# Performance work log

Measured on AMD Instinct MI355X. Metric: run time of the kernel, lower is better.

## Reference

```python
import jax, jax.numpy as jnp
import numpy as np

N = 50000
E = 800000
IN_F, HID, OUT_F = 512, 256, 64
KEEP = 0.5  # Dropout(0.5)


def setup_inputs() -> dict:
    key = jax.random.key(0)
    ks = jax.random.split(key, 7)
    X = jax.random.normal(ks[0], (N, IN_F), dtype=jnp.float32)
    # Xavier-uniform-style init for the two layer weights
    lim1 = float(np.sqrt(6.0 / (IN_F + HID)))
    lim2 = float(np.sqrt(6.0 / (HID + OUT_F)))
    W1 = jax.random.uniform(ks[1], (IN_F, HID), jnp.float32, -lim1, lim1)
    W2 = jax.random.uniform(ks[2], (HID, OUT_F), jnp.float32, -lim2, lim2)
    a_row = jnp.sort(jax.random.randint(ks[3], (E,), 0, N)).astype(jnp.int64)
    a_col = jax.random.randint(ks[4], (E,), 0, N).astype(jnp.int64)
    a_val = jax.random.uniform(ks[5], (E,), jnp.float32)
    drop_mask = jax.random.randint(ks[6], (N, HID), 0, 2).astype(jnp.int32)
    return {"X": X, "W1": W1, "W2": W2, "a_row": a_row, "a_col": a_col,
            "a_val": a_val, "drop_mask": drop_mask}


def _spmm(a_row, a_col, a_val, dense):
    # A @ dense where A is [N, N] sparse in COO form: gather + weighted segment-sum
    msgs = a_val[:, None] * dense[a_col]          # [E, d]
    return jax.ops.segment_sum(msgs, a_row, num_segments=N)


def reference(X, W1, W2, a_row, a_col, a_val, drop_mask):
    # layer 1: feature transform + neighbor aggregation
    h = _spmm(a_row, a_col, a_val, X @ W1)        # [N, HID]
    h = jax.nn.relu(h)
    h = h * drop_mask.astype(h.dtype) * (1.0 / KEEP)  # Dropout(0.5), train mode
    # layer 2
    out = _spmm(a_row, a_col, a_val, h @ W2)      # [N, OUT_F]
    return jax.nn.log_softmax(out, axis=1)
```

## Files before the change

### kernel.cpp

```cpp
#include <hip/hip_runtime.h>
#include <hip/hip_fp16.h>
#include <math.h>

#define NN   50000
#define EE   800000
#define INF  512
#define HIDF 256
#define OUTF 64
#define MTILES (NN/16)

using half8  = __attribute__((ext_vector_type(8))) _Float16;
using half2v = __attribute__((ext_vector_type(2))) _Float16;
using f32x4  = __attribute__((ext_vector_type(4))) float;

#if __has_builtin(__builtin_amdgcn_fdot2)
#define HAS_DOT2 1
#else
#define HAS_DOT2 0
#endif

__global__ void k_prep(const int* __restrict__ a_row, int* __restrict__ row_ptr,
                       const float* __restrict__ W1, _Float16* __restrict__ W1p,
                       const float* __restrict__ W2, _Float16* __restrict__ W2T){
  int b = blockIdx.x, tid = threadIdx.x;
  if (b < 196){
    int i = b * 256 + tid;
    if (i > NN) return;
    int lo = 0, hi = EE;
    while (lo < hi){ int mid = (lo + hi) >> 1; if (a_row[mid] < i) lo = mid + 1; else hi = mid; }
    row_ptr[i] = lo;
  } else if (b < 708){
    int idx = (b - 196) * 256 + tid;
    int k = idx >> 8, col = idx & 255;
    int kk = k >> 5, k2 = k & 31;
    W1p[((kk << 8) + col) * 32 + k2] = (_Float16)W1[idx];
  } else {
    int idx = (b - 708) * 256 + tid;
    int k = idx >> 6, n = idx & 63;
    W2T[n * HIDF + k] = (_Float16)W2[idx];
  }
}

__global__ __launch_bounds__(256, 4) void k_gemm1(const float* __restrict__ X,
                                                  const _Float16* __restrict__ W1p,
                                                  _Float16* __restrict__ XW1s){
  int wave = threadIdx.x >> 6, lane = threadIdx.x & 63;
  int l16 = lane & 15, quad = lane >> 4;
  int tile = blockIdx.x * 4 + wave;
  if (tile >= MTILES) return;
  int m0 = tile * 16;
  const float* arow = X + (size_t)(m0 + l16) * INF + quad * 8;

  f32x4 acc[16];
  #pragma unroll
  for (int t = 0; t < 16; t++) acc[t] = (f32x4){0.f,0.f,0.f,0.f};

  for (int kk = 0; kk < INF/32; kk++){
    const float4* ap = (const float4*)(arow + kk * 32);
    float4 a0 = ap[0], a1 = ap[1];
    half8 af;
    af[0]=(_Float16)a0.x; af[1]=(_Float16)a0.y; af[2]=(_Float16)a0.z; af[3]=(_Float16)a0.w;
    af[4]=(_Float16)a1.x; af[5]=(_Float16)a1.y; af[6]=(_Float16)a1.z; af[7]=(_Float16)a1.w;

    const _Float16* bchunk = W1p + kk * (256*32);
    #pragma unroll
    for (int nt = 0; nt < 16; nt++){
      half8 bf = *(const half8*)(bchunk + (nt*16 + l16) * 32 + quad * 8);
      acc[nt] = __builtin_amdgcn_mfma_f32_16x16x32_f16(af, bf, acc[nt], 0, 0, 0);
    }
  }
  #pragma unroll
  for (int nt = 0; nt < 16; nt++){
    int s = nt >> 1;
    _Float16* base = XW1s + (size_t)s * NN * 32 + (nt & 1) * 16 + l16;
    #pragma unroll
    for (int r = 0; r < 4; r++)
      base[(size_t)(m0 + quad*4 + r) * 32] = (_Float16)acc[nt][r];
  }
}

__global__ __launch_bounds__(256) void k_spmm1(const int* __restrict__ row_ptr,
                                               const int* __restrict__ a_col,
                                               const float* __restrict__ a_val,
                                               const _Float16* __restrict__ XW1s,
                                               const int* __restrict__ drop_mask,
                                               _Float16* __restrict__ hb){
  int s  = blockIdx.x & 7;
  int rg = blockIdx.x >> 3;
  int wave = threadIdx.x >> 6, lane = threadIdx.x & 63;
  int row_local = lane >> 4;
  int grp = (lane >> 2) & 3;
  int q   = lane & 3;
  int r = rg * 16 + wave * 4 + row_local;
  int es = row_ptr[r], ee = row_ptr[r+1];
  const _Float16* Xs = XW1s + (size_t)s * NN * 32 + q * 8;

  float acc[8] = {0,0,0,0,0,0,0,0};
  int i = es + grp;
  for (; i + 4 < ee; i += 8){
    float v0 = a_val[i];     int c0 = a_col[i];
    float v1 = a_val[i+4];   int c1 = a_col[i+4];
    int4 x0 = *(const int4*)(Xs + (size_t)c0 * 32);
    int4 x1 = *(const int4*)(Xs + (size_t)c1 * 32);
#if HAS_DOT2
    half2v vv = { (_Float16)v0, (_Float16)v1 };
    const int xs0[4] = {x0.x, x0.y, x0.z, x0.w};
    const int xs1[4] = {x1.x, x1.y, x1.z, x1.w};
    #pragma unroll
    for (int d = 0; d < 4; d++){
      int lo = __builtin_amdgcn_perm(xs1[d], xs0[d], 0x05040100);
      int hi = __builtin_amdgcn_perm(xs1[d], xs0[d], 0x07060302);
      acc[2*d]   = __builtin_amdgcn_fdot2(__builtin_bit_cast(half2v, lo), vv, acc[2*d],   false);
      acc[2*d+1] = __builtin_amdgcn_fdot2(__builtin_bit_cast(half2v, hi), vv, acc[2*d+1], false);
    }
#else
    const int xs0[4] = {x0.x, x0.y, x0.z, x0.w};
    const int xs1[4] = {x1.x, x1.y, x1.z, x1.w};
    #pragma unroll
    for (int d = 0; d < 4; d++){
      half2v h0 = __builtin_bit_cast(half2v, xs0[d]);
      half2v h1 = __builtin_bit_cast(half2v, xs1[d]);
      acc[2*d]   += v0 * (float)h0.x + v1 * (float)h1.x;
      acc[2*d+1] += v0 * (float)h0.y + v1 * (float)h1.y;
    }
#endif
  }
  for (; i < ee; i += 4){
    float v = a_val[i];  int c = a_col[i];
    int4 x = *(const int4*)(Xs + (size_t)c * 32);
    const int xs[4] = {x.x, x.y, x.z, x.w};
    #pragma unroll
    for (int d = 0; d < 4; d++){
      half2v h = __builtin_bit_cast(half2v, xs[d]);
      acc[2*d]   += v * (float)h.x;
      acc[2*d+1] += v * (float)h.y;
    }
  }
  #pragma unroll
  for (int j = 0; j < 8; j++){
    acc[j] += __shfl_xor(acc[j], 4);
    acc[j] += __shfl_xor(acc[j], 8);
  }
  if (grp == 0){
    const int* dm = drop_mask + (size_t)r * HIDF + s * 32 + q * 8;
    int4 d0 = *(const int4*)(dm);
    int4 d1 = *(const int4*)(dm + 4);
    half8 o;
    o[0] = (_Float16)(fmaxf(acc[0],0.f) * (float)d0.x * 2.0f);
    o[1] = (_Float16)(fmaxf(acc[1],0.f) * (float)d0.y * 2.0f);
    o[2] = (_Float16)(fmaxf(acc[2],0.f) * (float)d0.z * 2.0f);
    o[3] = (_Float16)(fmaxf(acc[3],0.f) * (float)d0.w * 2.0f);
    o[4] = (_Float16)(fmaxf(acc[4],0.f) * (float)d1.x * 2.0f);
    o[5] = (_Float16)(fmaxf(acc[5],0.f) * (float)d1.y * 2.0f);
    o[6] = (_Float16)(fmaxf(acc[6],0.f) * (float)d1.z * 2.0f);
    o[7] = (_Float16)(fmaxf(acc[7],0.f) * (float)d1.w * 2.0f);
    *(half8*)(hb + (size_t)r * HIDF + s * 32 + q * 8) = o;
  }
}

__global__ __launch_bounds__(256) void k_gemm2(const _Float16* __restrict__ A,
                                               const _Float16* __restrict__ BT,
                                               _Float16* __restrict__ HW2){
  int wave = threadIdx.x >> 6, lane = threadIdx.x & 63;
  int tile_m = blockIdx.x * 4 + wave;
  if (tile_m >= MTILES) return;
  int m0 = tile_m * 16, l16 = lane & 15, quad = lane >> 4;

  f32x4 acc[4];
  #pragma unroll
  for (int t = 0; t < 4; t++) acc[t] = (f32x4){0.f,0.f,0.f,0.f};

  const _Float16* ar = A + (size_t)(m0 + l16) * HIDF + quad * 8;
  for (int kk = 0; kk < HIDF/32; kk++){
    half8 af = *(const half8*)(ar + kk * 32);
    #pragma unroll
    for (int nt = 0; nt < 4; nt++){
      half8 bf = *(const half8*)(BT + (size_t)(nt*16 + l16) * HIDF + kk*32 + quad*8);
      acc[nt] = __builtin_amdgcn_mfma_f32_16x16x32_f16(af, bf, acc[nt], 0, 0, 0);
    }
  }
  #pragma unroll
  for (int nt = 0; nt < 4; nt++){
    int col = nt*16 + l16;
    #pragma unroll
    for (int r = 0; r < 4; r++)
      HW2[(size_t)(m0 + quad*4 + r) * OUTF + col] = (_Float16)acc[nt][r];
  }
}

__global__ __launch_bounds__(256) void k_spmm2_lsm(const int* __restrict__ row_ptr,
                                                   const int* __restrict__ a_col,
                                                   const float* __restrict__ a_val,
                                                   const _Float16* __restrict__ HW2,
                                                   float* __restrict__ out){
  int wave = threadIdx.x >> 6, lane = threadIdx.x & 63;
  int r = blockIdx.x * 4 + wave;
  int s = row_ptr[r], e = row_ptr[r+1];
  int g = lane >> 3;
  int q = lane & 7;
  float acc[8] = {0,0,0,0,0,0,0,0};

  int i = s + g;
  for (; i + 8 < e; i += 16){
    float v0 = a_val[i];     int c0 = a_col[i];
    float v1 = a_val[i+8];   int c1 = a_col[i+8];
    int4 x0 = *(const int4*)(HW2 + (size_t)c0 * OUTF + q * 8);
    int4 x1 = *(const int4*)(HW2 + (size_t)c1 * OUTF + q * 8);
#if HAS_DOT2
    half2v vv = { (_Float16)v0, (_Float16)v1 };
    const int xs0[4] = {x0.x, x0.y, x0.z, x0.w};
    const int xs1[4] = {x1.x, x1.y, x1.z, x1.w};
    #pragma unroll
    for (int d = 0; d < 4; d++){
      int lo = __builtin_amdgcn_perm(xs1[d], xs0[d], 0x05040100);
      int hi = __builtin_amdgcn_perm(xs1[d], xs0[d], 0x07060302);
      acc[2*d]   = __builtin_amdgcn_fdot2(__builtin_bit_cast(half2v, lo), vv, acc[2*d],   false);
      acc[2*d+1] = __builtin_amdgcn_fdot2(__builtin_bit_cast(half2v, hi), vv, acc[2*d+1], false);
    }
#else
    const int xs0[4] = {x0.x, x0.y, x0.z, x0.w};
    const int xs1[4] = {x1.x, x1.y, x1.z, x1.w};
    #pragma unroll
    for (int d = 0; d < 4; d++){
      half2v h0 = __builtin_bit_cast(half2v, xs0[d]);
      half2v h1 = __builtin_bit_cast(half2v, xs1[d]);
      acc[2*d]   += v0 * (float)h0.x + v1 * (float)h1.x;
      acc[2*d+1] += v0 * (float)h0.y + v1 * (float)h1.y;
    }
#endif
  }
  for (; i < e; i += 8){
    float v = a_val[i];  int c = a_col[i];
    int4 x = *(const int4*)(HW2 + (size_t)c * OUTF + q * 8);
    const int xs[4] = {x.x, x.y, x.z, x.w};
    #pragma unroll
    for (int d = 0; d < 4; d++){
      half2v h = __builtin_bit_cast(half2v, xs[d]);
      acc[2*d]   += v * (float)h.x;
      acc[2*d+1] += v * (float)h.y;
    }
  }
  #pragma unroll
  for (int j = 0; j < 8; j++){
    acc[j] += __shfl_xor(acc[j], 8);
    acc[j] += __shfl_xor(acc[j], 16);
    acc[j] += __shfl_xor(acc[j], 32);
  }
  float m = acc[0];
  #pragma unroll
  for (int j = 1; j < 8; j++) m = fmaxf(m, acc[j]);
  #pragma unroll
  for (int o = 1; o <= 4; o <<= 1) m = fmaxf(m, __shfl_xor(m, o));
  float ssum = 0.f;
  #pragma unroll
  for (int j = 0; j < 8; j++) ssum += expf(acc[j] - m);
  #pragma unroll
  for (int o = 1; o <= 4; o <<= 1) ssum += __shfl_xor(ssum, o);
  float ls = m + logf(ssum);
  if (g == 0){
    float4 o0 = { acc[0]-ls, acc[1]-ls, acc[2]-ls, acc[3]-ls };
    float4 o1 = { acc[4]-ls, acc[5]-ls, acc[6]-ls, acc[7]-ls };
    float* op = out + (size_t)r * OUTF + q * 8;
    *(float4*)(op)     = o0;
    *(float4*)(op + 4) = o1;
  }
}

extern "C" void kernel_launch(void* const* d_in, const int* in_sizes, int n_in,
                              void* d_out, int out_size, void* d_ws, size_t ws_size,
                              hipStream_t stream) {
  const float* X      = (const float*)d_in[0];
  const float* W1     = (const float*)d_in[1];
  const float* W2     = (const float*)d_in[2];
  const int*   a_row  = (const int*)d_in[3];
  const int*   a_col  = (const int*)d_in[4];
  const float* a_val  = (const float*)d_in[5];
  const int*   drop   = (const int*)d_in[6];
  float*       out    = (float*)d_out;

  char* ws = (char*)d_ws;
  int*       row_ptr = (int*)      (ws);
  _Float16*  W1p     = (_Float16*)(ws + 200704);
  _Float16*  W2T     = (_Float16*)(ws + 462848);
  _Float16*  XW1s    = (_Float16*)(ws + 495616);
  _Float16*  hb      = (_Float16*)(ws + 26095616);
  _Float16*  HW2     = (_Float16*)(ws + 51695616);

  k_prep<<<772, 256, 0, stream>>>(a_row, row_ptr, W1, W1p, W2, W2T);
  k_gemm1<<<(MTILES + 3)/4, 256, 0, stream>>>(X, W1p, XW1s);
  k_spmm1<<<8 * (NN/16), 256, 0, stream>>>(row_ptr, a_col, a_val, XW1s, drop, hb);
  k_gemm2<<<(MTILES + 3)/4, 256, 0, stream>>>(hb, W2T, HW2);
  k_spmm2_lsm<<<NN/4, 256, 0, stream>>>(row_ptr, a_col, a_val, HW2, out);
}
```

Before: 368.7 us.

## Pack col/val edges and map one row per lane group in SpMM kernels

Adds an int2 array that packs a_col and a_val per edge, built in the prep kernel, so each edge costs one 8-byte load instead of two separate loads. Both SpMM kernels now give each row to a small lane group (4 lanes in spmm1, 8 in spmm2) that walks all of that row's edges serially with a 4-way unrolled loop. This removes the cross-group shuffle reductions and packs more rows per block. The trade-offs are an extra prep pass over the edges, lanes idling within a wave when row lengths differ, and less coalescing of edge loads since neighbouring lane groups read different rows.

```diff
diff --git a/kernel.cpp b/kernel.cpp
--- a/kernel.cpp
+++ b/kernel.cpp
@@ -21,7 +21,9 @@
 
 __global__ void k_prep(const int* __restrict__ a_row, int* __restrict__ row_ptr,
                        const float* __restrict__ W1, _Float16* __restrict__ W1p,
-                       const float* __restrict__ W2, _Float16* __restrict__ W2T){
+                       const float* __restrict__ W2, _Float16* __restrict__ W2T,
+                       const int* __restrict__ a_col, const float* __restrict__ a_val,
+                       int2* __restrict__ epk){
   int b = blockIdx.x, tid = threadIdx.x;
   if (b < 196){
     int i = b * 256 + tid;
@@ -34,10 +36,14 @@
     int k = idx >> 8, col = idx & 255;
     int kk = k >> 5, k2 = k & 31;
     W1p[((kk << 8) + col) * 32 + k2] = (_Float16)W1[idx];
-  } else {
+  } else if (b < 772){
     int idx = (b - 708) * 256 + tid;
     int k = idx >> 6, n = idx & 63;
     W2T[n * HIDF + k] = (_Float16)W2[idx];
+  } else {
+    int idx = (b - 772) * 256 + tid;
+    int2 e; e.x = a_col[idx]; e.y = __builtin_bit_cast(int, a_val[idx]);
+    epk[idx] = e;
   }
 }
 
@@ -80,54 +86,70 @@
 }
 
 __global__ __launch_bounds__(256) void k_spmm1(const int* __restrict__ row_ptr,
-                                               const int* __restrict__ a_col,
-                                               const float* __restrict__ a_val,
+                                               const int2* __restrict__ epk,
                                                const _Float16* __restrict__ XW1s,
                                                const int* __restrict__ drop_mask,
                                                _Float16* __restrict__ hb){
   int s  = blockIdx.x & 7;
-  int rg = blockIdx.x >> 3;
-  int wave = threadIdx.x >> 6, lane = threadIdx.x & 63;
-  int row_local = lane >> 4;
-  int grp = (lane >> 2) & 3;
-  int q   = lane & 3;
-  int r = rg * 16 + wave * 4 + row_local;
-  int es = row_ptr[r], ee = row_ptr[r+1];
+  int bg = blockIdx.x >> 3;
+  int lane = threadIdx.x & 63, wave = threadIdx.x >> 6;
+  int rl = lane >> 2;
+  int q  = lane & 3;
+  int r = bg * 64 + wave * 16 + rl;
+  bool valid = r < NN;
+  int rc = valid ? r : NN - 1;
+  int es = row_ptr[rc], ee = row_ptr[rc + 1];
+  if (!valid) ee = es;
   const _Float16* Xs = XW1s + (size_t)s * NN * 32 + q * 8;
 
   float acc[8] = {0,0,0,0,0,0,0,0};
-  int i = es + grp;
-  for (; i + 4 < ee; i += 8){
-    float v0 = a_val[i];     int c0 = a_col[i];
-    float v1 = a_val[i+4];   int c1 = a_col[i+4];
-    int4 x0 = *(const int4*)(Xs + (size_t)c0 * 32);
-    int4 x1 = *(const int4*)(Xs + (size_t)c1 * 32);
+  int i = es;
+  for (; i + 3 < ee; i += 4){
+    int2 e0 = epk[i], e1 = epk[i+1], e2 = epk[i+2], e3 = epk[i+3];
+    int4 x0 = *(const int4*)(Xs + (size_t)e0.x * 32);
+    int4 x1 = *(const int4*)(Xs + (size_t)e1.x * 32);
+    int4 x2 = *(const int4*)(Xs + (size_t)e2.x * 32);
+    int4 x3 = *(const int4*)(Xs + (size_t)e3.x * 32);
+    float v0 = __builtin_bit_cast(float, e0.y);
+    float v1 = __builtin_bit_cast(float, e1.y);
+    float v2 = __builtin_bit_cast(float, e2.y);
+    float v3 = __builtin_bit_cast(float, e3.y);
 #if HAS_DOT2
-    half2v vv = { (_Float16)v0, (_Float16)v1 };
+    half2v va = { (_Float16)v0, (_Float16)v1 };
+    half2v vb = { (_Float16)v2, (_Float16)v3 };
     const int xs0[4] = {x0.x, x0.y, x0.z, x0.w};
     const int xs1[4] = {x1.x, x1.y, x1.z, x1.w};
+    const int xs2[4] = {x2.x, x2.y, x2.z, x2.w};
+    const int xs3[4] = {x3.x, x3.y, x3.z, x3.w};
     #pragma unroll
     for (int d = 0; d < 4; d++){
-      int lo = __builtin_amdgcn_perm(xs1[d], xs0[d], 0x05040100);
-      int hi = __builtin_amdgcn_perm(xs1[d], xs0[d], 0x07060302);
-      acc[2*d]   = __builtin_amdgcn_fdot2(__builtin_bit_cast(half2v, lo), vv, acc[2*d],   false);
-      acc[2*d+1] = __builtin_amdgcn_fdot2(__builtin_bit_cast(half2v, hi), vv, acc[2*d+1], false);
+      int loa = __builtin_amdgcn_perm(xs1[d], xs0[d], 0x05040100);
+      int hia = __builtin_amdgcn_perm(xs1[d], xs0[d], 0x07060302);
+      int lob = __builtin_amdgcn_perm(xs3[d], xs2[d], 0x05040100);
+      int hib = __builtin_amdgcn_perm(xs3[d], xs2[d], 0x07060302);
+      acc[2*d]   = __builtin_amdgcn_fdot2(__builtin_bit_cast(half2v, loa), va, acc[2*d],   false);
+      acc[2*d+1] = __builtin_amdgcn_fdot2(__builtin_bit_cast(half2v, hia), va, acc[2*d+1], false);
+      acc[2*d]   = __builtin_amdgcn_fdot2(__builtin_bit_cast(half2v, lob), vb, acc[2*d],   false);
+      acc[2*d+1] = __builtin_amdgcn_fdot2(__builtin_bit_cast(half2v, hib), vb, acc[2*d+1], false);
     }
 #else
-    const int xs0[4] = {x0.x, x0.y, x0.z, x0.w};
-    const int xs1[4] = {x1.x, x1.y, x1.z, x1.w};
-    #pragma unroll
-    for (int d = 0; d < 4; d++){
-      half2v h0 = __builtin_bit_cast(half2v, xs0[d]);
-      half2v h1 = __builtin_bit_cast(half2v, xs1[d]);
-      acc[2*d]   += v0 * (float)h0.x + v1 * (float)h1.x;
-      acc[2*d+1] += v0 * (float)h0.y + v1 * (float)h1.y;
-    }
+    const int xsA[4][4] = {{x0.x,x0.y,x0.z,x0.w},{x1.x,x1.y,x1.z,x1.w},
+                           {x2.x,x2.y,x2.z,x2.w},{x3.x,x3.y,x3.z,x3.w}};
+    const float vA[4] = {v0,v1,v2,v3};
+    #pragma unroll
+    for (int k = 0; k < 4; k++)
+      #pragma unroll
+      for (int d = 0; d < 4; d++){
+        half2v h = __builtin_bit_cast(half2v, xsA[k][d]);
+        acc[2*d]   += vA[k] * (float)h.x;
+        acc[2*d+1] += vA[k] * (float)h.y;
+      }
 #endif
   }
-  for (; i < ee; i += 4){
-    float v = a_val[i];  int c = a_col[i];
-    int4 x = *(const int4*)(Xs + (size_t)c * 32);
+  for (; i < ee; i++){
+    int2 e = epk[i];
+    float v = __builtin_bit_cast(float, e.y);
+    int4 x = *(const int4*)(Xs + (size_t)e.x * 32);
     const int xs[4] = {x.x, x.y, x.z, x.w};
     #pragma unroll
     for (int d = 0; d < 4; d++){
@@ -136,12 +158,7 @@
       acc[2*d+1] += v * (float)h.y;
     }
   }
-  #pragma unroll
-  for (int j = 0; j < 8; j++){
-    acc[j] += __shfl_xor(acc[j], 4);
-    acc[j] += __shfl_xor(acc[j], 8);
-  }
-  if (grp == 0){
+  if (valid){
     const int* dm = drop_mask + (size_t)r * HIDF + s * 32 + q * 8;
     int4 d0 = *(const int4*)(dm);
     int4 d1 = *(const int4*)(dm + 4);
@@ -189,49 +206,67 @@
 }
 
 __global__ __launch_bounds__(256) void k_spmm2_lsm(const int* __restrict__ row_ptr,
-                                                   const int* __restrict__ a_col,
-                                                   const float* __restrict__ a_val,
+                                                   const int2* __restrict__ epk,
                                                    const _Float16* __restrict__ HW2,
                                                    float* __restrict__ out){
-  int wave = threadIdx.x >> 6, lane = threadIdx.x & 63;
-  int r = blockIdx.x * 4 + wave;
-  int s = row_ptr[r], e = row_ptr[r+1];
-  int g = lane >> 3;
-  int q = lane & 7;
+  int lane = threadIdx.x & 63, wave = threadIdx.x >> 6;
+  int rl = lane >> 3;
+  int q  = lane & 7;
+  int r = blockIdx.x * 32 + wave * 8 + rl;
+  bool valid = r < NN;
+  int rc = valid ? r : NN - 1;
+  int es = row_ptr[rc], ee = row_ptr[rc + 1];
+  if (!valid) ee = es;
+  const _Float16* Hs = HW2 + q * 8;
+
   float acc[8] = {0,0,0,0,0,0,0,0};
-
-  int i = s + g;
-  for (; i + 8 < e; i += 16){
-    float v0 = a_val[i];     int c0 = a_col[i];
-    float v1 = a_val[i+8];   int c1 = a_col[i+8];
-    int4 x0 = *(const int4*)(HW2 + (size_t)c0 * OUTF + q * 8);
-    int4 x1 = *(const int4*)(HW2 + (size_t)c1 * OUTF + q * 8);
+  int i = es;
+  for (; i + 3 < ee; i += 4){
+    int2 e0 = epk[i], e1 = epk[i+1], e2 = epk[i+2], e3 = epk[i+3];
+    int4 x0 = *(const int4*)(Hs + (size_t)e0.x * OUTF);
+    int4 x1 = *(const int4*)(Hs + (size_t)e1.x * OUTF);
+    int4 x2 = *(const int4*)(Hs + (size_t)e2.x * OUTF);
+    int4 x3 = *(const int4*)(Hs + (size_t)e3.x * OUTF);
+    float v0 = __builtin_bit_cast(float, e0.y);
+    float v1 = __builtin_bit_cast(float, e1.y);
+    float v2 = __builtin_bit_cast(float, e2.y);
+    float v3 = __builtin_bit_cast(float, e3.y);
 #if HAS_DOT2
-    half2v vv = { (_Float16)v0, (_Float16)v1 };
+    half2v va = { (_Float16)v0, (_Float16)v1 };
+    half2v vb = { (_Float16)v2, (_Float16)v3 };
     const int xs0[4] = {x0.x, x0.y, x0.z, x0.w};
     const int xs1[4] = {x1.x, x1.y, x1.z, x1.w};
+    const int xs2[4] = {x2.x, x2.y, x2.z, x2.w};
+    const int xs3[4] = {x3.x, x3.y, x3.z, x3.w};
     #pragma unroll
     for (int d = 0; d < 4; d++){
-      int lo = __builtin_amdgcn_perm(xs1[d], xs0[d], 0x05040100);
-      int hi = __builtin_amdgcn_perm(xs1[d], xs0[d], 0x07060302);
-      acc[2*d]   = __builtin_amdgcn_fdot2(__builtin_bit_cast(half2v, lo), vv, acc[2*d],   false);
-      acc[2*d+1] = __builtin_amdgcn_fdot2(__builtin_bit_cast(half2v, hi), vv, acc[2*d+1], false);
+      int loa = __builtin_amdgcn_perm(xs1[d], xs0[d], 0x05040100);
+      int hia = __builtin_amdgcn_perm(xs1[d], xs0[d], 0x07060302);
+      int lob = __builtin_amdgcn_perm(xs3[d], xs2[d], 0x05040100);
+      int hib = __builtin_amdgcn_perm(xs3[d], xs2[d], 0x07060302);
+      acc[2*d]   = __builtin_amdgcn_fdot2(__builtin_bit_cast(half2v, loa), va, acc[2*d],   false);
+      acc[2*d+1] = __builtin_amdgcn_fdot2(__builtin_bit_cast(half2v, hia), va, acc[2*d+1], false);
+      acc[2*d]   = __builtin_amdgcn_fdot2(__builtin_bit_cast(half2v, lob), vb, acc[2*d],   false);
+      acc[2*d+1] = __builtin_amdgcn_fdot2(__builtin_bit_cast(half2v, hib), vb, acc[2*d+1], false);
     }
 #else
-    const int xs0[4] = {x0.x, x0.y, x0.z, x0.w};
-    const int xs1[4] = {x1.x, x1.y, x1.z, x1.w};
-    #pragma unroll
-    for (int d = 0; d < 4; d++){
-      half2v h0 = __builtin_bit_cast(half2v, xs0[d]);
-      half2v h1 = __builtin_bit_cast(half2v, xs1[d]);
-      acc[2*d]   += v0 * (float)h0.x + v1 * (float)h1.x;
-      acc[2*d+1] += v0 * (float)h0.y + v1 * (float)h1.y;
-    }
+    const int xsA[4][4] = {{x0.x,x0.y,x0.z,x0.w},{x1.x,x1.y,x1.z,x1.w},
+                           {x2.x,x2.y,x2.z,x2.w},{x3.x,x3.y,x3.z,x3.w}};
+    const float vA[4] = {v0,v1,v2,v3};
+    #pragma unroll
+    for (int k = 0; k < 4; k++)
+      #pragma unroll
+      for (int d = 0; d < 4; d++){
+        half2v h = __builtin_bit_cast(half2v, xsA[k][d]);
+        acc[2*d]   += vA[k] * (float)h.x;
+        acc[2*d+1] += vA[k] * (float)h.y;
+      }
 #endif
   }
-  for (; i < e; i += 8){
-    float v = a_val[i];  int c = a_col[i];
-    int4 x = *(const int4*)(HW2 + (size_t)c * OUTF + q * 8);
+  for (; i < ee; i++){
+    int2 e = epk[i];
+    float v = __builtin_bit_cast(float, e.y);
+    int4 x = *(const int4*)(Hs + (size_t)e.x * OUTF);
     const int xs[4] = {x.x, x.y, x.z, x.w};
     #pragma unroll
     for (int d = 0; d < 4; d++){
@@ -240,12 +275,6 @@
       acc[2*d+1] += v * (float)h.y;
     }
   }
-  #pragma unroll
-  for (int j = 0; j < 8; j++){
-    acc[j] += __shfl_xor(acc[j], 8);
-    acc[j] += __shfl_xor(acc[j], 16);
-    acc[j] += __shfl_xor(acc[j], 32);
-  }
   float m = acc[0];
   #pragma unroll
   for (int j = 1; j < 8; j++) m = fmaxf(m, acc[j]);
@@ -257,7 +286,7 @@
   #pragma unroll
   for (int o = 1; o <= 4; o <<= 1) ssum += __shfl_xor(ssum, o);
   float ls = m + logf(ssum);
-  if (g == 0){
+  if (valid){
     float4 o0 = { acc[0]-ls, acc[1]-ls, acc[2]-ls, acc[3]-ls };
     float4 o1 = { acc[4]-ls, acc[5]-ls, acc[6]-ls, acc[7]-ls };
     float* op = out + (size_t)r * OUTF + q * 8;
@@ -285,10 +314,11 @@
   _Float16*  XW1s    = (_Float16*)(ws + 495616);
   _Float16*  hb      = (_Float16*)(ws + 26095616);
   _Float16*  HW2     = (_Float16*)(ws + 51695616);
-
-  k_prep<<<772, 256, 0, stream>>>(a_row, row_ptr, W1, W1p, W2, W2T);
+  int2*      epk     = (int2*)    (ws + 58095616);
+
+  k_prep<<<3897, 256, 0, stream>>>(a_row, row_ptr, W1, W1p, W2, W2T, a_col, a_val, epk);
   k_gemm1<<<(MTILES + 3)/4, 256, 0, stream>>>(X, W1p, XW1s);
-  k_spmm1<<<8 * (NN/16), 256, 0, stream>>>(row_ptr, a_col, a_val, XW1s, drop, hb);
+  k_spmm1<<<8 * ((NN + 63)/64), 256, 0, stream>>>(row_ptr, epk, XW1s, drop, hb);
   k_gemm2<<<(MTILES + 3)/4, 256, 0, stream>>>(hb, W2T, HW2);
-  k_spmm2_lsm<<<NN/4, 256, 0, stream>>>(row_ptr, a_col, a_val, HW2, out);
-}
+  k_spmm2_lsm<<<(NN + 31)/32, 256, 0, stream>>>(row_ptr, epk, HW2, out);
+}
```

Result: faster. 361.3 us (-2.0%).
